# Kernel optimization log

Measured on AMD Instinct MI355X. Metric: run time of the kernel, lower is better.

The kernel has to match this reference:

```python
import jax, jax.numpy as jnp
import numpy as np

WX, WY = 32, 32
N = WX * WY                      # 1024 tokens
TOKEN_DIM = 1024
QKV = 512
H = 8
HD = QKV // H                    # 64
TOPK = 32
B = 64
NUM_UNIQUE = (2 * WX - 1) * (2 * WY - 1)  # 3969 unique relative offsets
LN_EPS = 1e-5


def _make_rel_idx():
    # identical to torch create_positional_biases: lexicographic unique index of (dx, dy)
    ix = np.arange(N) // WY
    iy = np.arange(N) % WY
    dx = ix[:, None] - ix[None, :]
    dy = iy[:, None] - iy[None, :]
    rel = (dx + WX - 1) * (2 * WY - 1) + (dy + WY - 1)
    return jnp.asarray(rel, dtype=jnp.int32)  # [N, N]


def _layernorm(x, g, b):
    m = jnp.mean(x, axis=-1, keepdims=True)
    v = jnp.mean(jnp.square(x - m), axis=-1, keepdims=True)
    return (x - m) * jax.lax.rsqrt(v + LN_EPS) * g + b


def setup_inputs() -> dict:
    key = jax.random.key(0)
    ks = jax.random.split(key, 12)
    s = 0.02
    return {
        "x": jax.random.normal(ks[0], (B, N, TOKEN_DIM), jnp.float32),
        "scorer_w": jax.random.normal(ks[1], (1, TOKEN_DIM), jnp.float32) * s,
        "scorer_b": jnp.zeros((1,), jnp.float32),
        "ln_g": jnp.ones((TOKEN_DIM,), jnp.float32),
        "ln_b": jnp.zeros((TOKEN_DIM,), jnp.float32),
        "qk_w": jax.random.normal(ks[2], (QKV, TOKEN_DIM), jnp.float32) * s,
        "qk_b": jnp.zeros((QKV,), jnp.float32),
        "v_w": jax.random.normal(ks[3], (QKV, TOKEN_DIM), jnp.float32) * s,
        "v_b": jnp.zeros((QKV,), jnp.float32),
        "skip_w": jax.random.normal(ks[4], (QKV, TOKEN_DIM), jnp.float32) * s,
        "skip_b": jnp.zeros((QKV,), jnp.float32),
        "out_w": jax.random.normal(ks[5], (QKV, QKV), jnp.float32) * s,
        "out_b": jnp.zeros((QKV,), jnp.float32),
        "fc_w": jax.random.normal(ks[6], (2, QKV), jnp.float32) * s,
        "fc_b": jnp.zeros((2,), jnp.float32),
        "unique_bias": jax.random.normal(ks[7], (NUM_UNIQUE,), jnp.float32) * s,
        "rel_idx": _make_rel_idx(),
    }


def reference(x, scorer_w, scorer_b, ln_g, ln_b, qk_w, qk_b, v_w, v_b,
              skip_w, skip_b, out_w, out_b, fc_w, fc_b, unique_bias, rel_idx):
    # token selection (eval path: argmax of relevance logits)
    logits = jnp.einsum('bnd,od->bno', x, scorer_w)[..., 0] + scorer_b[0]  # [B, N]
    sel_idx = jnp.argmax(logits, axis=-1)                                   # [B]
    sel_tok = x[jnp.arange(B), sel_idx]                                     # [B, D]

    x_n = _layernorm(x, ln_g, ln_b)
    s_n = _layernorm(sel_tok, ln_g, ln_b)

    value = (jnp.einsum('bnd,qd->bnq', x_n, v_w) + v_b).reshape(B, N, H, HD).transpose(0, 2, 1, 3)  # [B,H,N,hd]
    key_t = (jnp.einsum('bnd,qd->bnq', x_n, qk_w) + qk_b).reshape(B, N, H, HD).transpose(0, 2, 1, 3)
    query = (s_n @ qk_w.T + qk_b).reshape(B, H, HD)                         # [B,H,hd]

    attn = jnp.einsum('bhd,bhnd->bhn', query, key_t) / jnp.sqrt(jnp.float32(HD))  # [B,H,N]
    bias = unique_bias[rel_idx[sel_idx]]                                    # gather: [B, N]
    attn = jax.nn.softmax(attn + bias[:, None, :], axis=-1)

    # top-k sparsification + renormalization
    _, topk_idx = jax.lax.top_k(attn, TOPK)                                 # [B,H,K]
    mask = jax.nn.one_hot(topk_idx, N, dtype=attn.dtype).sum(axis=-2)       # [B,H,N] 0/1
    attn = attn * mask
    attn = attn / (attn.sum(axis=-1, keepdims=True) + 1e-9)

    y = jnp.einsum('bhn,bhnd->bhd', attn, value).reshape(B, QKV)            # [B, QKV]
    skip = sel_tok @ skip_w.T + skip_b
    y = jax.nn.relu(y + skip)
    # dropout is identity in eval mode
    y = y @ out_w.T + out_b
    y = y @ fc_w.T + fc_b
    return y  # [B, 2]
```

## Files before the change

kernel.cpp:

```cpp
#include <hip/hip_runtime.h>
#include <hip/hip_bf16.h>
#include <math.h>

#define WX 32
#define WY 32
#define NTOK 1024
#define TD 1024
#define QKV 512
#define NH 8
#define HD 64
#define TOPK 32
#define BB 64

__device__ __forceinline__ float wred_sum(float v){
  #pragma unroll
  for (int o=32;o;o>>=1) v += __shfl_xor(v,o,64);
  return v;
}
__device__ __forceinline__ float wred_max(float v){
  #pragma unroll
  for (int o=32;o;o>>=1) v = fmaxf(v, __shfl_xor(v,o,64));
  return v;
}
__device__ __forceinline__ float dot4f(float4 a, float4 b){
  return a.x*b.x + a.y*b.y + a.z*b.z + a.w*b.w;
}

__global__ __launch_bounds__(256) void k1_stats(
    const float* __restrict__ x, const float* __restrict__ sw, const float* __restrict__ sb,
    float* __restrict__ mean, float* __restrict__ rstd, float* __restrict__ logit){
  int wave = threadIdx.x >> 6, lane = threadIdx.x & 63;
  int tok = blockIdx.x*4 + wave;
  const float4* xp = (const float4*)(x + (size_t)tok*TD);
  const float4* sp = (const float4*)sw;
  float s1=0.f, s2=0.f, sd=0.f;
  #pragma unroll
  for (int j=0;j<4;j++){
    float4 v = xp[lane + j*64];
    float4 w = sp[lane + j*64];
    s1 += v.x+v.y+v.z+v.w;
    s2 += v.x*v.x + v.y*v.y + v.z*v.z + v.w*v.w;
    sd += dot4f(v,w);
  }
  s1 = wred_sum(s1); s2 = wred_sum(s2); sd = wred_sum(sd);
  if (lane==0){
    float m = s1*(1.f/1024.f);
    float var = s2*(1.f/1024.f) - m*m;
    mean[tok] = m;
    rstd[tok] = rsqrtf(var + 1e-5f);
    logit[tok] = sd + sb[0];
  }
}

__global__ __launch_bounds__(256) void k2_prep(
    const float* __restrict__ x, const float* __restrict__ logit,
    const float* __restrict__ mean, const float* __restrict__ rstd,
    const float* __restrict__ lng, const float* __restrict__ lnb,
    const float* __restrict__ qkw, const float* __restrict__ qkb,
    const int* __restrict__ relIdx, const float* __restrict__ ub,
    int* __restrict__ selI, float* __restrict__ gu8,
    float* __restrict__ Aw, float* __restrict__ C0w, float* __restrict__ biasArr){
  __shared__ float sn[TD];
  __shared__ float qs[HD];
  __shared__ float red[256];
  __shared__ float redV[4]; __shared__ int redI[4];
  __shared__ int sel_s;
  int b = blockIdx.x >> 3, h = blockIdx.x & 7;
  int t = threadIdx.x, lane = t&63, wave = t>>6;

  const float* lg = logit + b*NTOK;
  float bv = -INFINITY; int bi = 0;
  #pragma unroll
  for (int j=0;j<4;j++){ int idx = t*4+j; float v = lg[idx]; if (v > bv){ bv=v; bi=idx; } }
  #pragma unroll
  for (int o=32;o;o>>=1){
    float vv = __shfl_xor(bv,o,64); int ii = __shfl_xor(bi,o,64);
    if (vv > bv || (vv == bv && ii < bi)){ bv=vv; bi=ii; }
  }
  if (lane==0){ redV[wave]=bv; redI[wave]=bi; }
  __syncthreads();
  if (t==0){
    float v = redV[0]; int i = redI[0];
    for (int w=1; w<4; w++){ if (redV[w] > v || (redV[w]==v && redI[w]<i)){ v=redV[w]; i=redI[w]; } }
    sel_s = i;
    if (h==0) selI[b] = i;
  }
  __syncthreads();
  int sel = sel_s;
  float m = mean[b*NTOK+sel], r = rstd[b*NTOK+sel];
  float4 g4 = ((const float4*)lng)[t];
  float4 b4 = ((const float4*)lnb)[t];
  {
    float4 xv = ((const float4*)(x + ((size_t)b*NTOK + sel)*TD))[t];
    float4 s4;
    s4.x = (xv.x-m)*r*g4.x + b4.x;
    s4.y = (xv.y-m)*r*g4.y + b4.y;
    s4.z = (xv.z-m)*r*g4.z + b4.z;
    s4.w = (xv.w-m)*r*g4.w + b4.w;
    ((float4*)sn)[t] = s4;
  }
  __syncthreads();
  {
    int row = t>>2, part = t&3;
    const float4* wr = (const float4*)(qkw + (size_t)(h*HD+row)*TD + part*256);
    const float4* xp = ((const float4*)sn) + part*64;
    float a0 = 0.f, a1 = 0.f;
    #pragma unroll 4
    for (int j=0;j<64;j+=2){ a0 += dot4f(wr[j], xp[j]); a1 += dot4f(wr[j+1], xp[j+1]); }
    red[t] = a0 + a1;
  }
  __syncthreads();
  if (t < HD) qs[t] = red[t*4]+red[t*4+1]+red[t*4+2]+red[t*4+3] + qkb[h*HD+t];
  __syncthreads();
  float4 accE = make_float4(0.f,0.f,0.f,0.f);
  float4 accO = make_float4(0.f,0.f,0.f,0.f);
  #pragma unroll 4
  for (int c=0;c<HD;c+=2){
    float q0 = qs[c], q1 = qs[c+1];
    float4 w0 = ((const float4*)(qkw + (size_t)(h*HD+c)*TD))[t];
    float4 w1 = ((const float4*)(qkw + (size_t)(h*HD+c+1)*TD))[t];
    accE.x += q0*w0.x; accE.y += q0*w0.y; accE.z += q0*w0.z; accE.w += q0*w0.w;
    accO.x += q1*w1.x; accO.y += q1*w1.y; accO.z += q1*w1.z; accO.w += q1*w1.w;
  }
  float4 acc;
  acc.x = accE.x+accO.x; acc.y = accE.y+accO.y; acc.z = accE.z+accO.z; acc.w = accE.w+accO.w;
  {
    float4 gu;
    gu.x = acc.x*g4.x*0.125f; gu.y = acc.y*g4.y*0.125f;
    gu.z = acc.z*g4.z*0.125f; gu.w = acc.w*g4.w*0.125f;
    ((float4*)(gu8 + ((size_t)(b*NH+h))*TD))[t] = gu;
  }
  float su_p = g4.x*acc.x + g4.y*acc.y + g4.z*acc.z + g4.w*acc.w;
  float bu_p = b4.x*acc.x + b4.y*acc.y + b4.z*acc.z + b4.w*acc.w;
  su_p = wred_sum(su_p); bu_p = wred_sum(bu_p);
  if (lane==0){ red[wave] = su_p; red[8+wave] = bu_p; }
  if (wave==0){
    float qb_p = qs[lane]*qkb[h*HD+lane];
    qb_p = wred_sum(qb_p);
    if (lane==0) red[16] = qb_p;
  }
  __syncthreads();
  if (t==0){
    float s  = red[0]+red[1]+red[2]+red[3];
    float bb = red[8]+red[9]+red[10]+red[11];
    Aw[b*NH+h]  = s*0.125f;
    C0w[b*NH+h] = (bb + red[16])*0.125f;
  }
  if (h==0){
    const int* rp = relIdx + (size_t)sel*NTOK;
    #pragma unroll
    for (int j=0;j<4;j++){
      int n = t*4+j;
      biasArr[b*NTOK+n] = ub[rp[n]];
    }
  }
}

__global__ __launch_bounds__(256) void k3_attn(
    const float* __restrict__ x, const float* __restrict__ mean, const float* __restrict__ rstd,
    const float* __restrict__ gu8, const float* __restrict__ Aw, const float* __restrict__ C0w,
    const float* __restrict__ biasArr, float* __restrict__ attL){
  int b = blockIdx.x >> 4;
  int chunk = blockIdx.x & 15;
  int lane = threadIdx.x & 63, wave = threadIdx.x >> 6;

  const float4* gp = (const float4*)(gu8 + (size_t)b*NH*TD);
  float4 G[NH][4];
  #pragma unroll
  for (int h=0;h<NH;h++)
    #pragma unroll
    for (int j=0;j<4;j++)
      G[h][j] = gp[h*256 + j*64 + lane];
  float Ah[NH], Ch[NH];
  #pragma unroll
  for (int h=0;h<NH;h++){ Ah[h] = Aw[b*NH+h]; Ch[h] = C0w[b*NH+h]; }

  const int base = chunk*64 + wave*16;
  float4 cur[4];
  {
    const float4* xp = (const float4*)(x + ((size_t)b*NTOK + base)*TD);
    #pragma unroll
    for (int j=0;j<4;j++) cur[j] = xp[j*64 + lane];
  }
  for (int i=0;i<16;i++){
    int n = base + i;
    int tok = b*NTOK + n;
    float4 nxt[4];
    if (i < 15){
      const float4* xp = (const float4*)(x + (size_t)(tok+1)*TD);
      #pragma unroll
      for (int j=0;j<4;j++) nxt[j] = xp[j*64 + lane];
    }
    float m = mean[tok], r = rstd[tok], bias = biasArr[b*NTOK+n];
    float s[NH];
    #pragma unroll
    for (int h=0;h<NH;h++){
      float a = dot4f(cur[0],G[h][0]) + dot4f(cur[1],G[h][1])
              + dot4f(cur[2],G[h][2]) + dot4f(cur[3],G[h][3]);
      s[h] = wred_sum(a);
    }
    #pragma unroll
    for (int h=0;h<NH;h++){
      if (lane == h)
        attL[((size_t)b*NH+h)*NTOK + n] = r*s[h] - r*m*Ah[h] + Ch[h] + bias;
    }
    if (i < 15){
      #pragma unroll
      for (int j=0;j<4;j++) cur[j] = nxt[j];
    }
  }
}

__global__ __launch_bounds__(256) void k4_topkv(
    const float* __restrict__ x, const float* __restrict__ mean, const float* __restrict__ rstd,
    const float* __restrict__ lng, const float* __restrict__ lnb,
    const float* __restrict__ vw, const float* __restrict__ vb,
    const float* __restrict__ attL, const int* __restrict__ selI,
    const float* __restrict__ skw, const float* __restrict__ skb,
    float* __restrict__ t1ws){
  __shared__ float redf[4];
  __shared__ float cV[128]; __shared__ int cI[128];
  __shared__ float selV[TOPK]; __shared__ int selIs[TOPK];
  __shared__ float aa[TOPK]; __shared__ float am[TOPK];
  __shared__ float xbar[TD];
  __shared__ float red2[256];
  int b = blockIdx.x >> 3, h = blockIdx.x & 7;
  int t = threadIdx.x, lane = t&63, wave = t>>6;

  float4 Lv = ((const float4*)(attL + ((size_t)b*NH + h)*NTOK))[t];
  float lm = fmaxf(fmaxf(Lv.x,Lv.y), fmaxf(Lv.z,Lv.w));
  lm = wred_max(lm);
  if (lane==0) redf[wave] = lm;
  __syncthreads();
  float maxL = fmaxf(fmaxf(redf[0],redf[1]), fmaxf(redf[2],redf[3]));
  __syncthreads();
  float ev[4];
  ev[0] = __expf(Lv.x - maxL); ev[1] = __expf(Lv.y - maxL);
  ev[2] = __expf(Lv.z - maxL); ev[3] = __expf(Lv.w - maxL);
  float zp = ev[0]+ev[1]+ev[2]+ev[3];
  zp = wred_sum(zp);
  if (lane==0) redf[wave] = zp;
  __syncthreads();
  float Z = redf[0]+redf[1]+redf[2]+redf[3];

  for (int k=0;k<TOPK;k++){
    float bv = -1.f; int bi = 1<<20;
    #pragma unroll
    for (int j=0;j<4;j++){ if (ev[j] > bv){ bv = ev[j]; bi = t*4+j; } }
    #pragma unroll
    for (int o=32;o;o>>=1){
      float vv = __shfl_xor(bv,o,64); int ii = __shfl_xor(bi,o,64);
      if (vv > bv || (vv == bv && ii < bi)){ bv=vv; bi=ii; }
    }
    #pragma unroll
    for (int j=0;j<4;j++){ if (bi == t*4+j) ev[j] = -1.f; }
    if (lane==0){ cV[wave*TOPK+k] = bv; cI[wave*TOPK+k] = bi; }
  }
  __syncthreads();
  float selContrib = 0.f;
  if (t < 128){
    float v = cV[t]; int idx = cI[t];
    int rank = 0;
    #pragma unroll 8
    for (int j0=0;j0<32;j0++){
      float4 v4 = ((float4*)cV)[j0];
      int4  i4 = ((int4*)cI)[j0];
      rank += (v4.x > v) || (v4.x==v && i4.x<idx);
      rank += (v4.y > v) || (v4.y==v && i4.y<idx);
      rank += (v4.z > v) || (v4.z==v && i4.z<idx);
      rank += (v4.w > v) || (v4.w==v && i4.w<idx);
    }
    if (rank < TOPK){ selV[rank]=v; selIs[rank]=idx; selContrib = v; }
  }
  float Sp = wred_sum(selContrib);
  if (lane==0) redf[wave] = Sp;
  __syncthreads();
  float S = redf[0]+redf[1]+redf[2]+redf[3];
  float denom = S + 1e-9f*Z;
  float W = S/denom;
  if (t < TOPK){
    int ni = selIs[t];
    float w = selV[t]/denom;
    float a = w * rstd[b*NTOK+ni];
    aa[t] = a; am[t] = a*mean[b*NTOK+ni];
  }
  __syncthreads();
  float c = 0.f;
  #pragma unroll
  for (int k=0;k<TOPK;k++) c += am[k];

  float4 acc = make_float4(0.f,0.f,0.f,0.f);
  for (int k=0;k<TOPK;k++){
    float a = aa[k];
    float4 xv = ((const float4*)(x + ((size_t)b*NTOK + selIs[k])*TD))[t];
    acc.x += a*xv.x; acc.y += a*xv.y; acc.z += a*xv.z; acc.w += a*xv.w;
  }
  float4 g4 = ((const float4*)lng)[t];
  float4 b4 = ((const float4*)lnb)[t];
  float4 xb;
  xb.x = g4.x*(acc.x - c) + b4.x*W;
  xb.y = g4.y*(acc.y - c) + b4.y*W;
  xb.z = g4.z*(acc.z - c) + b4.z*W;
  xb.w = g4.w*(acc.w - c) + b4.w*W;
  ((float4*)xbar)[t] = xb;
  __syncthreads();

  int co = t >> 2, part = t & 3;
  int row = h*HD + co;
  {
    const float4* vp = (const float4*)(vw + (size_t)row*TD + part*256);
    const float4* xp2 = ((const float4*)xbar) + part*64;
    float a0 = 0.f, a1 = 0.f;
    #pragma unroll 4
    for (int j=0;j<64;j+=2){ a0 += dot4f(vp[j], xp2[j]); a1 += dot4f(vp[j+1], xp2[j+1]); }
    red2[t] = a0 + a1;
  }
  int sel = selI[b];
  float4 xs4 = ((const float4*)(x + ((size_t)b*NTOK + sel)*TD))[t];
  __syncthreads();
  float ypart = 0.f;
  if (part==0) ypart = red2[t]+red2[t+1]+red2[t+2]+red2[t+3] + vb[row]*W;
  ((float4*)xbar)[t] = xs4;
  __syncthreads();
  {
    const float4* wr = (const float4*)(skw + (size_t)row*TD + part*256);
    const float4* xp2 = ((const float4*)xbar) + part*64;
    float a0 = 0.f, a1 = 0.f;
    #pragma unroll 4
    for (int j=0;j<64;j+=2){ a0 += dot4f(wr[j], xp2[j]); a1 += dot4f(wr[j+1], xp2[j+1]); }
    red2[t] = a0 + a1;
  }
  __syncthreads();
  if (part==0){
    float skip = red2[t]+red2[t+1]+red2[t+2]+red2[t+3] + skb[row];
    t1ws[b*QKV + row] = fmaxf(ypart + skip, 0.f);
  }
}

__global__ __launch_bounds__(256) void k5bc(
    const float* __restrict__ t1ws, const float* __restrict__ ow,
    const float* __restrict__ ob, const float* __restrict__ fcw,
    const float* __restrict__ fcb, float* __restrict__ out){
  __shared__ float t1s[QKV];
  __shared__ float t2s[QKV];
  __shared__ float redA[4]; __shared__ float redB[4];
  int b = blockIdx.x, t = threadIdx.x, lane = t&63, wave = t>>6;
  if (t < 128) ((float4*)t1s)[t] = ((const float4*)(t1ws + (size_t)b*QKV))[t];
  __syncthreads();
  int r0 = 2*t;
  {
    const float4* w0 = (const float4*)(ow + (size_t)r0*QKV);
    const float4* w1 = (const float4*)(ow + (size_t)(r0+1)*QKV);
    float a0 = 0.f, a1 = 0.f;
    #pragma unroll 8
    for (int j=0;j<128;j++){ float4 x4 = ((float4*)t1s)[j]; a0 += dot4f(w0[j], x4); a1 += dot4f(w1[j], x4); }
    t2s[r0]   = a0 + ob[r0];
    t2s[r0+1] = a1 + ob[r0+1];
  }
  __syncthreads();
  float v0 = t2s[r0], v1 = t2s[r0+1];
  float p0 = v0*fcw[r0] + v1*fcw[r0+1];
  float p1 = v0*fcw[QKV+r0] + v1*fcw[QKV+r0+1];
  p0 = wred_sum(p0); p1 = wred_sum(p1);
  if (lane==0){ redA[wave]=p0; redB[wave]=p1; }
  __syncthreads();
  if (t==0){
    out[b*2+0] = redA[0]+redA[1]+redA[2]+redA[3] + fcb[0];
    out[b*2+1] = redB[0]+redB[1]+redB[2]+redB[3] + fcb[1];
  }
}

extern "C" void kernel_launch(void* const* d_in, const int* in_sizes, int n_in,
                              void* d_out, int out_size, void* d_ws, size_t ws_size,
                              hipStream_t stream) {
  const float* x   = (const float*)d_in[0];
  const float* sw  = (const float*)d_in[1];
  const float* sb  = (const float*)d_in[2];
  const float* lng = (const float*)d_in[3];
  const float* lnb = (const float*)d_in[4];
  const float* qkw = (const float*)d_in[5];
  const float* qkb = (const float*)d_in[6];
  const float* vw  = (const float*)d_in[7];
  const float* vb  = (const float*)d_in[8];
  const float* skw = (const float*)d_in[9];
  const float* skb = (const float*)d_in[10];
  const float* ow  = (const float*)d_in[11];
  const float* ob  = (const float*)d_in[12];
  const float* fcw = (const float*)d_in[13];
  const float* fcb = (const float*)d_in[14];
  const float* ub  = (const float*)d_in[15];
  const int*   ri  = (const int*)d_in[16];
  float* out = (float*)d_out;

  float* wsf     = (float*)d_ws;
  float* logit   = wsf;
  float* mean    = wsf + 65536;
  float* rstd    = wsf + 131072;
  int*   selI    = (int*)(wsf + 196608);
  float* gu8     = wsf + 196672;
  float* Aw      = wsf + 720960;
  float* C0w     = wsf + 721472;
  float* biasArr = wsf + 721984;
  float* attL    = wsf + 787520;
  float* t1ws    = wsf + 1311808;

  k1_stats<<<16384, 256, 0, stream>>>(x, sw, sb, mean, rstd, logit);
  k2_prep<<<BB*NH, 256, 0, stream>>>(x, logit, mean, rstd, lng, lnb, qkw, qkb,
                                     ri, ub, selI, gu8, Aw, C0w, biasArr);
  k3_attn<<<BB*16, 256, 0, stream>>>(x, mean, rstd, gu8, Aw, C0w, biasArr, attL);
  k4_topkv<<<BB*NH, 256, 0, stream>>>(x, mean, rstd, lng, lnb, vw, vb, attL,
                                      selI, skw, skb, t1ws);
  k5bc<<<BB, 256, 0, stream>>>(t1ws, ow, ob, fcw, fcb, out);
}
```

Baseline: 577.0 us.

## Prefetch tokens in stats kernel, stage attention logits in LDS, fuse V/skip dots

The stats kernel now has each wave handle four tokens, with the next row prefetched into registers and the scorer weights loaded once per wave. The grid shrinks to match. The attention kernel stages per-head logits in shared memory so it writes coalesced 64-wide rows instead of scattered single-lane stores. The top-k/value kernel loads the selected token early into its own shared buffer and fuses the V-projection and skip-projection dot products into one loop, removing two barriers and a second reduction pass. These cut uncoalesced global stores and synchronization in exchange for more shared memory and register pressure.

```diff
diff --git a/kernel.cpp b/kernel.cpp
--- a/kernel.cpp
+++ b/kernel.cpp
@@ -30,25 +30,40 @@
     const float* __restrict__ x, const float* __restrict__ sw, const float* __restrict__ sb,
     float* __restrict__ mean, float* __restrict__ rstd, float* __restrict__ logit){
   int wave = threadIdx.x >> 6, lane = threadIdx.x & 63;
-  int tok = blockIdx.x*4 + wave;
-  const float4* xp = (const float4*)(x + (size_t)tok*TD);
+  int tok0 = blockIdx.x*16 + wave*4;
   const float4* sp = (const float4*)sw;
-  float s1=0.f, s2=0.f, sd=0.f;
-  #pragma unroll
-  for (int j=0;j<4;j++){
-    float4 v = xp[lane + j*64];
-    float4 w = sp[lane + j*64];
-    s1 += v.x+v.y+v.z+v.w;
-    s2 += v.x*v.x + v.y*v.y + v.z*v.z + v.w*v.w;
-    sd += dot4f(v,w);
-  }
-  s1 = wred_sum(s1); s2 = wred_sum(s2); sd = wred_sum(sd);
-  if (lane==0){
-    float m = s1*(1.f/1024.f);
-    float var = s2*(1.f/1024.f) - m*m;
-    mean[tok] = m;
-    rstd[tok] = rsqrtf(var + 1e-5f);
-    logit[tok] = sd + sb[0];
+  float4 w0 = sp[lane], w1 = sp[64+lane], w2 = sp[128+lane], w3 = sp[192+lane];
+  float sb0 = sb[0];
+  float4 cur[4];
+  {
+    const float4* xp = (const float4*)(x + (size_t)tok0*TD);
+    cur[0]=xp[lane]; cur[1]=xp[64+lane]; cur[2]=xp[128+lane]; cur[3]=xp[192+lane];
+  }
+  #pragma unroll
+  for (int i=0;i<4;i++){
+    int tok = tok0 + i;
+    float4 nxt[4];
+    if (i<3){
+      const float4* xp = (const float4*)(x + (size_t)(tok+1)*TD);
+      nxt[0]=xp[lane]; nxt[1]=xp[64+lane]; nxt[2]=xp[128+lane]; nxt[3]=xp[192+lane];
+    }
+    float s1=0.f, s2=0.f, sd=0.f;
+    s1 += cur[0].x+cur[0].y+cur[0].z+cur[0].w;  s2 += dot4f(cur[0],cur[0]);  sd += dot4f(cur[0],w0);
+    s1 += cur[1].x+cur[1].y+cur[1].z+cur[1].w;  s2 += dot4f(cur[1],cur[1]);  sd += dot4f(cur[1],w1);
+    s1 += cur[2].x+cur[2].y+cur[2].z+cur[2].w;  s2 += dot4f(cur[2],cur[2]);  sd += dot4f(cur[2],w2);
+    s1 += cur[3].x+cur[3].y+cur[3].z+cur[3].w;  s2 += dot4f(cur[3],cur[3]);  sd += dot4f(cur[3],w3);
+    s1 = wred_sum(s1); s2 = wred_sum(s2); sd = wred_sum(sd);
+    if (lane==0){
+      float m = s1*(1.f/1024.f);
+      float var = s2*(1.f/1024.f) - m*m;
+      mean[tok] = m;
+      rstd[tok] = rsqrtf(var + 1e-5f);
+      logit[tok] = sd + sb0;
+    }
+    if (i<3){
+      #pragma unroll
+      for (int j=0;j<4;j++) cur[j] = nxt[j];
+    }
   }
 }
 
@@ -160,6 +175,7 @@
     const float* __restrict__ x, const float* __restrict__ mean, const float* __restrict__ rstd,
     const float* __restrict__ gu8, const float* __restrict__ Aw, const float* __restrict__ C0w,
     const float* __restrict__ biasArr, float* __restrict__ attL){
+  __shared__ float sL[NH*65];
   int b = blockIdx.x >> 4;
   int chunk = blockIdx.x & 15;
   int lane = threadIdx.x & 63, wave = threadIdx.x >> 6;
@@ -202,12 +218,18 @@
     #pragma unroll
     for (int h=0;h<NH;h++){
       if (lane == h)
-        attL[((size_t)b*NH+h)*NTOK + n] = r*s[h] - r*m*Ah[h] + Ch[h] + bias;
+        sL[h*65 + wave*16 + i] = r*s[h] - r*m*Ah[h] + Ch[h] + bias;
     }
     if (i < 15){
       #pragma unroll
       for (int j=0;j<4;j++) cur[j] = nxt[j];
     }
+  }
+  __syncthreads();
+  #pragma unroll
+  for (int hh=0; hh<2; hh++){
+    int h = wave + hh*4;
+    attL[((size_t)b*NH+h)*NTOK + chunk*64 + lane] = sL[h*65 + lane];
   }
 }
 
@@ -223,9 +245,13 @@
   __shared__ float selV[TOPK]; __shared__ int selIs[TOPK];
   __shared__ float aa[TOPK]; __shared__ float am[TOPK];
   __shared__ float xbar[TD];
+  __shared__ float xs[TD];
   __shared__ float red2[256];
   int b = blockIdx.x >> 3, h = blockIdx.x & 7;
   int t = threadIdx.x, lane = t&63, wave = t>>6;
+
+  int sel = selI[b];
+  ((float4*)xs)[t] = ((const float4*)(x + ((size_t)b*NTOK + sel)*TD))[t];
 
   float4 Lv = ((const float4*)(attL + ((size_t)b*NH + h)*NTOK))[t];
   float lm = fmaxf(fmaxf(Lv.x,Lv.y), fmaxf(Lv.z,Lv.w));
@@ -242,6 +268,7 @@
   if (lane==0) redf[wave] = zp;
   __syncthreads();
   float Z = redf[0]+redf[1]+redf[2]+redf[3];
+  __syncthreads();
 
   for (int k=0;k<TOPK;k++){
     float bv = -1.f; int bi = 1<<20;
@@ -309,31 +336,21 @@
   int row = h*HD + co;
   {
     const float4* vp = (const float4*)(vw + (size_t)row*TD + part*256);
-    const float4* xp2 = ((const float4*)xbar) + part*64;
+    const float4* kp = (const float4*)(skw + (size_t)row*TD + part*256);
+    const float4* xb2 = ((const float4*)xbar) + part*64;
+    const float4* xs2 = ((const float4*)xs) + part*64;
     float a0 = 0.f, a1 = 0.f;
     #pragma unroll 4
-    for (int j=0;j<64;j+=2){ a0 += dot4f(vp[j], xp2[j]); a1 += dot4f(vp[j+1], xp2[j+1]); }
+    for (int j=0;j<64;j+=2){
+      a0 += dot4f(vp[j], xb2[j]) + dot4f(kp[j], xs2[j]);
+      a1 += dot4f(vp[j+1], xb2[j+1]) + dot4f(kp[j+1], xs2[j+1]);
+    }
     red2[t] = a0 + a1;
   }
-  int sel = selI[b];
-  float4 xs4 = ((const float4*)(x + ((size_t)b*NTOK + sel)*TD))[t];
-  __syncthreads();
-  float ypart = 0.f;
-  if (part==0) ypart = red2[t]+red2[t+1]+red2[t+2]+red2[t+3] + vb[row]*W;
-  ((float4*)xbar)[t] = xs4;
-  __syncthreads();
-  {
-    const float4* wr = (const float4*)(skw + (size_t)row*TD + part*256);
-    const float4* xp2 = ((const float4*)xbar) + part*64;
-    float a0 = 0.f, a1 = 0.f;
-    #pragma unroll 4
-    for (int j=0;j<64;j+=2){ a0 += dot4f(wr[j], xp2[j]); a1 += dot4f(wr[j+1], xp2[j+1]); }
-    red2[t] = a0 + a1;
-  }
   __syncthreads();
   if (part==0){
-    float skip = red2[t]+red2[t+1]+red2[t+2]+red2[t+3] + skb[row];
-    t1ws[b*QKV + row] = fmaxf(ypart + skip, 0.f);
+    float y = red2[t] + red2[t+1] + red2[t+2] + red2[t+3] + vb[row]*W + skb[row];
+    t1ws[b*QKV + row] = fmaxf(y, 0.f);
   }
 }
 
@@ -404,7 +421,7 @@
   float* attL    = wsf + 787520;
   float* t1ws    = wsf + 1311808;
 
-  k1_stats<<<16384, 256, 0, stream>>>(x, sw, sb, mean, rstd, logit);
+  k1_stats<<<4096, 256, 0, stream>>>(x, sw, sb, mean, rstd, logit);
   k2_prep<<<BB*NH, 256, 0, stream>>>(x, logit, mean, rstd, lng, lnb, qkw, qkb,
                                      ri, ub, selI, gu8, Aw, C0w, biasArr);
   k3_attn<<<BB*16, 256, 0, stream>>>(x, mean, rstd, gu8, Aw, C0w, biasArr, attL);
```

New measurement: 573.0 us. Within noise of the previous version (-0.7%).
